# Performance work log

Hardware: AMD Instinct MI355X
Metric: run time of the kernel (lower is better)

## Reference

```python
import jax, jax.numpy as jnp
import numpy as np

DIM = 128
E = 400000
G = 512


def setup_inputs() -> dict:
    key = jax.random.key(0)
    ks = jax.random.split(key, 9)
    src = jax.random.normal(ks[0], (E, DIM), dtype=jnp.float32)
    dest = jax.random.normal(ks[1], (E, DIM), dtype=jnp.float32)
    edge_attr = jax.random.normal(ks[2], (E, DIM), dtype=jnp.float32)
    u = jax.random.normal(ks[3], (G, DIM), dtype=jnp.float32)
    batch = jnp.sort(jax.random.randint(ks[4], (E,), 0, G, dtype=jnp.int64))
    # MLP params: Linear(4*dim, dim) -> ReLU -> Linear(dim, dim)
    s1 = 1.0 / np.sqrt(4 * DIM)
    s2 = 1.0 / np.sqrt(DIM)
    W1 = jax.random.uniform(ks[5], (4 * DIM, DIM), minval=-s1, maxval=s1, dtype=jnp.float32)
    b1 = jax.random.uniform(ks[6], (DIM,), minval=-s1, maxval=s1, dtype=jnp.float32)
    W2 = jax.random.uniform(ks[7], (DIM, DIM), minval=-s2, maxval=s2, dtype=jnp.float32)
    b2 = jax.random.uniform(ks[8], (DIM,), minval=-s2, maxval=s2, dtype=jnp.float32)
    return {"src": src, "dest": dest, "edge_attr": edge_attr, "u": u,
            "batch": batch, "W1": W1, "b1": b1, "W2": W2, "b2": b2}


def reference(src, dest, edge_attr, u, batch, W1, b1, W2, b2):
    # gather global state per edge, concat 4 blocks -> [E, 4*dim]
    comb = jnp.concatenate([src, dest, edge_attr, u[batch]], axis=1)
    h = jax.nn.relu(comb @ W1 + b1)
    return h @ W2 + b2
```

## Files before the change

kernel.cpp:

```cpp
#include <hip/hip_runtime.h>

#define DIM 128

typedef __attribute__((ext_vector_type(8))) short short8;
typedef __attribute__((ext_vector_type(4))) float f32x4;

__device__ __forceinline__ unsigned short f2bf(float f) {
    union { float f; unsigned u; } v; v.f = f;
    unsigned u = v.u;
    return (unsigned short)((u + 0x7FFFu + ((u >> 16) & 1u)) >> 16);
}

__device__ __forceinline__ short8 cvt8(f32x4 lo, f32x4 hi) {
    short8 r;
    r[0] = (short)f2bf(lo[0]); r[1] = (short)f2bf(lo[1]);
    r[2] = (short)f2bf(lo[2]); r[3] = (short)f2bf(lo[3]);
    r[4] = (short)f2bf(hi[0]); r[5] = (short)f2bf(hi[1]);
    r[6] = (short)f2bf(hi[2]); r[7] = (short)f2bf(hi[3]);
    return r;
}

__global__ void prep_weights(const float* __restrict__ W1, const float* __restrict__ W2,
                             unsigned short* __restrict__ W1t, unsigned short* __restrict__ W2t) {
    int tid = blockIdx.x * blockDim.x + threadIdx.x;
    if (tid < 512 * 128) {
        int n = tid >> 9;
        int k = tid & 511;
        W1t[tid] = f2bf(W1[k * 128 + n]);
    } else if (tid < 512 * 128 + 128 * 128) {
        int t = tid - 512 * 128;
        int n = t >> 7;
        int k = t & 127;
        W2t[t] = f2bf(W2[k * 128 + n]);
    }
}

__device__ __forceinline__ void chunk_gemm(const float* p0, const float* p1,
                                           const unsigned short* __restrict__ wchunk,
                                           int quad, int l16, f32x4 acc[2][8]) {
#pragma unroll
    for (int s = 0; s < 4; ++s) {
        const int kl = s * 32 + quad * 8;
        f32x4 a0lo = *(const f32x4*)(p0 + kl);
        f32x4 a0hi = *(const f32x4*)(p0 + kl + 4);
        f32x4 a1lo = *(const f32x4*)(p1 + kl);
        f32x4 a1hi = *(const f32x4*)(p1 + kl + 4);
        short8 a0 = cvt8(a0lo, a0hi);
        short8 a1 = cvt8(a1lo, a1hi);
#pragma unroll
        for (int nt = 0; nt < 8; ++nt) {
            short8 b = *(const short8*)(wchunk + (nt * 16 + l16) * 512 + kl);
            acc[0][nt] = __builtin_amdgcn_mfma_f32_16x16x32_bf16(a0, b, acc[0][nt], 0, 0, 0);
            acc[1][nt] = __builtin_amdgcn_mfma_f32_16x16x32_bf16(a1, b, acc[1][nt], 0, 0, 0);
        }
    }
}

__global__ __launch_bounds__(256, 2)
void megnet_edge(const float* __restrict__ src, const float* __restrict__ dst,
                 const float* __restrict__ edge_attr, const float* __restrict__ u,
                 const int* __restrict__ batch,
                 const unsigned short* __restrict__ W1t, const unsigned short* __restrict__ W2t,
                 const float* __restrict__ b1, const float* __restrict__ b2,
                 float* __restrict__ out, int E) {
    __shared__ unsigned char lds_raw[4 * 32 * 256];

    const int tid  = threadIdx.x;
    const int wave = tid >> 6;
    const int lane = tid & 63;
    const int quad = lane >> 4;
    const int l16  = lane & 15;

    const long rowBase = (long)blockIdx.x * 128 + wave * 32;
    if (rowBase >= E) return;

    float b1r[8], b2r[8];
#pragma unroll
    for (int nt = 0; nt < 8; ++nt) {
        b1r[nt] = b1[nt * 16 + l16];
        b2r[nt] = b2[nt * 16 + l16];
    }

    const long ar0 = rowBase + l16;
    const long ar1 = rowBase + 16 + l16;
    const int ub0 = batch[ar0];
    const int ub1 = batch[ar1];

    f32x4 acc[2][8];
#pragma unroll
    for (int mt = 0; mt < 2; ++mt)
#pragma unroll
        for (int nt = 0; nt < 8; ++nt) acc[mt][nt] = (f32x4)0.0f;

    chunk_gemm(src + ar0 * DIM,       src + ar1 * DIM,       W1t + 0 * 128, quad, l16, acc);
    chunk_gemm(dst + ar0 * DIM,       dst + ar1 * DIM,       W1t + 1 * 128, quad, l16, acc);
    chunk_gemm(edge_attr + ar0 * DIM, edge_attr + ar1 * DIM, W1t + 2 * 128, quad, l16, acc);
    chunk_gemm(u + (long)ub0 * DIM,   u + (long)ub1 * DIM,   W1t + 3 * 128, quad, l16, acc);

    unsigned char* myLds = lds_raw + wave * 32 * 256;
#pragma unroll
    for (int mt = 0; mt < 2; ++mt)
#pragma unroll
        for (int nt = 0; nt < 8; ++nt)
#pragma unroll
            for (int r = 0; r < 4; ++r) {
                const int lr = mt * 16 + quad * 4 + r;
                const int cc = nt * 16 + l16;
                float h = acc[mt][nt][r] + b1r[nt];
                h = h > 0.0f ? h : 0.0f;
                const int g = (cc >> 3) ^ (lr & 7);
                *(unsigned short*)(myLds + lr * 256 + g * 16 + (cc & 7) * 2) = f2bf(h);
            }
    __syncthreads();

    f32x4 acc2[2][8];
#pragma unroll
    for (int mt = 0; mt < 2; ++mt)
#pragma unroll
        for (int nt = 0; nt < 8; ++nt) acc2[mt][nt] = (f32x4)0.0f;

#pragma unroll
    for (int s = 0; s < 4; ++s) {
        const int kl = s * 32 + quad * 8;
        const int g  = kl >> 3;
        const int lr0 = l16;
        const int lr1 = 16 + l16;
        short8 a0 = *(const short8*)(myLds + lr0 * 256 + ((g ^ (lr0 & 7)) * 16));
        short8 a1 = *(const short8*)(myLds + lr1 * 256 + ((g ^ (lr1 & 7)) * 16));
#pragma unroll
        for (int nt = 0; nt < 8; ++nt) {
            short8 b = *(const short8*)(W2t + (nt * 16 + l16) * 128 + kl);
            acc2[0][nt] = __builtin_amdgcn_mfma_f32_16x16x32_bf16(a0, b, acc2[0][nt], 0, 0, 0);
            acc2[1][nt] = __builtin_amdgcn_mfma_f32_16x16x32_bf16(a1, b, acc2[1][nt], 0, 0, 0);
        }
    }

#pragma unroll
    for (int mt = 0; mt < 2; ++mt)
#pragma unroll
        for (int nt = 0; nt < 8; ++nt)
#pragma unroll
            for (int r = 0; r < 4; ++r) {
                const long row = rowBase + mt * 16 + quad * 4 + r;
                const int col = nt * 16 + l16;
                out[row * DIM + col] = acc2[mt][nt][r] + b2r[nt];
            }
}

extern "C" void kernel_launch(void* const* d_in, const int* in_sizes, int n_in,
                              void* d_out, int out_size, void* d_ws, size_t ws_size,
                              hipStream_t stream) {
    const float* src       = (const float*)d_in[0];
    const float* dst       = (const float*)d_in[1];
    const float* edge_attr = (const float*)d_in[2];
    const float* u         = (const float*)d_in[3];
    const int*   batch     = (const int*)d_in[4];
    const float* W1        = (const float*)d_in[5];
    const float* b1        = (const float*)d_in[6];
    const float* W2        = (const float*)d_in[7];
    const float* b2        = (const float*)d_in[8];
    float* out             = (float*)d_out;

    unsigned short* W1t = (unsigned short*)d_ws;
    unsigned short* W2t = W1t + 512 * 128;

    const int E = in_sizes[0] / DIM;

    prep_weights<<<(512 * 128 + 128 * 128 + 255) / 256, 256, 0, stream>>>(W1, W2, W1t, W2t);
    megnet_edge<<<(E + 127) / 128, 256, 0, stream>>>(src, dst, edge_attr, u, batch,
                                                     W1t, W2t, b1, b2, out, E);
}
```

Measured before the change: 800.3 us.

## Software-pipeline activation and weight loads across GEMM chunks, drop block barrier

Restructures the first GEMM so the next input chunk's fp32 rows are prefetched into registers while the current chunk is converted and multiplied. Weight fragments are double-buffered one k-step ahead in both GEMMs. Because each wave only reads its own LDS region, the block-wide __syncthreads is replaced with a wave-local lgkmcnt wait. Bias loads are moved later to ease register pressure. The extra register buffers may raise VGPR use and risk spills under the 2-blocks-per-SIMD launch bound.

```diff
diff --git a/kernel.cpp b/kernel.cpp
--- a/kernel.cpp
+++ b/kernel.cpp
@@ -35,27 +35,6 @@
     }
 }
 
-__device__ __forceinline__ void chunk_gemm(const float* p0, const float* p1,
-                                           const unsigned short* __restrict__ wchunk,
-                                           int quad, int l16, f32x4 acc[2][8]) {
-#pragma unroll
-    for (int s = 0; s < 4; ++s) {
-        const int kl = s * 32 + quad * 8;
-        f32x4 a0lo = *(const f32x4*)(p0 + kl);
-        f32x4 a0hi = *(const f32x4*)(p0 + kl + 4);
-        f32x4 a1lo = *(const f32x4*)(p1 + kl);
-        f32x4 a1hi = *(const f32x4*)(p1 + kl + 4);
-        short8 a0 = cvt8(a0lo, a0hi);
-        short8 a1 = cvt8(a1lo, a1hi);
-#pragma unroll
-        for (int nt = 0; nt < 8; ++nt) {
-            short8 b = *(const short8*)(wchunk + (nt * 16 + l16) * 512 + kl);
-            acc[0][nt] = __builtin_amdgcn_mfma_f32_16x16x32_bf16(a0, b, acc[0][nt], 0, 0, 0);
-            acc[1][nt] = __builtin_amdgcn_mfma_f32_16x16x32_bf16(a1, b, acc[1][nt], 0, 0, 0);
-        }
-    }
-}
-
 __global__ __launch_bounds__(256, 2)
 void megnet_edge(const float* __restrict__ src, const float* __restrict__ dst,
                  const float* __restrict__ edge_attr, const float* __restrict__ u,
@@ -74,28 +53,79 @@
     const long rowBase = (long)blockIdx.x * 128 + wave * 32;
     if (rowBase >= E) return;
 
-    float b1r[8], b2r[8];
-#pragma unroll
-    for (int nt = 0; nt < 8; ++nt) {
-        b1r[nt] = b1[nt * 16 + l16];
-        b2r[nt] = b2[nt * 16 + l16];
-    }
-
     const long ar0 = rowBase + l16;
-    const long ar1 = rowBase + 16 + l16;
+    const long ar1 = ar0 + 16;
     const int ub0 = batch[ar0];
     const int ub1 = batch[ar1];
 
+    const float* rp0[4] = { src + ar0 * DIM, dst + ar0 * DIM, edge_attr + ar0 * DIM, u + (long)ub0 * DIM };
+    const float* rp1[4] = { src + ar1 * DIM, dst + ar1 * DIM, edge_attr + ar1 * DIM, u + (long)ub1 * DIM };
+
+    const int koff = quad * 8;
+
     f32x4 acc[2][8];
 #pragma unroll
     for (int mt = 0; mt < 2; ++mt)
 #pragma unroll
         for (int nt = 0; nt < 8; ++nt) acc[mt][nt] = (f32x4)0.0f;
 
-    chunk_gemm(src + ar0 * DIM,       src + ar1 * DIM,       W1t + 0 * 128, quad, l16, acc);
-    chunk_gemm(dst + ar0 * DIM,       dst + ar1 * DIM,       W1t + 1 * 128, quad, l16, acc);
-    chunk_gemm(edge_attr + ar0 * DIM, edge_attr + ar1 * DIM, W1t + 2 * 128, quad, l16, acc);
-    chunk_gemm(u + (long)ub0 * DIM,   u + (long)ub1 * DIM,   W1t + 3 * 128, quad, l16, acc);
+    f32x4 raw0[8], raw1[8];
+#pragma unroll
+    for (int j = 0; j < 8; ++j) {
+        const int off = (j >> 1) * 32 + koff + (j & 1) * 4;
+        raw0[j] = *(const f32x4*)(rp0[0] + off);
+        raw1[j] = *(const f32x4*)(rp1[0] + off);
+    }
+
+#pragma unroll
+    for (int c = 0; c < 4; ++c) {
+        short8 a0[4], a1[4];
+#pragma unroll
+        for (int s = 0; s < 4; ++s) a0[s] = cvt8(raw0[2 * s], raw0[2 * s + 1]);
+        if (c < 3) {
+#pragma unroll
+            for (int j = 0; j < 8; ++j) {
+                const int off = (j >> 1) * 32 + koff + (j & 1) * 4;
+                raw0[j] = *(const f32x4*)(rp0[c + 1] + off);
+            }
+        }
+#pragma unroll
+        for (int s = 0; s < 4; ++s) a1[s] = cvt8(raw1[2 * s], raw1[2 * s + 1]);
+        if (c < 3) {
+#pragma unroll
+            for (int j = 0; j < 8; ++j) {
+                const int off = (j >> 1) * 32 + koff + (j & 1) * 4;
+                raw1[j] = *(const f32x4*)(rp1[c + 1] + off);
+            }
+        }
+
+        const unsigned short* wc = W1t + c * 128;
+        short8 bn[8];
+#pragma unroll
+        for (int nt = 0; nt < 8; ++nt)
+            bn[nt] = *(const short8*)(wc + (nt * 16 + l16) * 512 + koff);
+
+#pragma unroll
+        for (int s = 0; s < 4; ++s) {
+            short8 bc[8];
+#pragma unroll
+            for (int nt = 0; nt < 8; ++nt) bc[nt] = bn[nt];
+            if (s < 3) {
+#pragma unroll
+                for (int nt = 0; nt < 8; ++nt)
+                    bn[nt] = *(const short8*)(wc + (nt * 16 + l16) * 512 + (s + 1) * 32 + koff);
+            }
+#pragma unroll
+            for (int nt = 0; nt < 8; ++nt) {
+                acc[0][nt] = __builtin_amdgcn_mfma_f32_16x16x32_bf16(a0[s], bc[nt], acc[0][nt], 0, 0, 0);
+                acc[1][nt] = __builtin_amdgcn_mfma_f32_16x16x32_bf16(a1[s], bc[nt], acc[1][nt], 0, 0, 0);
+            }
+        }
+    }
+
+    float b1r[8];
+#pragma unroll
+    for (int nt = 0; nt < 8; ++nt) b1r[nt] = b1[nt * 16 + l16];
 
     unsigned char* myLds = lds_raw + wave * 32 * 256;
 #pragma unroll
@@ -111,7 +141,7 @@
                 const int g = (cc >> 3) ^ (lr & 7);
                 *(unsigned short*)(myLds + lr * 256 + g * 16 + (cc & 7) * 2) = f2bf(h);
             }
-    __syncthreads();
+    asm volatile("s_waitcnt lgkmcnt(0)" ::: "memory");
 
     f32x4 acc2[2][8];
 #pragma unroll
@@ -119,21 +149,41 @@
 #pragma unroll
         for (int nt = 0; nt < 8; ++nt) acc2[mt][nt] = (f32x4)0.0f;
 
+    short8 ha0[4], ha1[4];
 #pragma unroll
     for (int s = 0; s < 4; ++s) {
-        const int kl = s * 32 + quad * 8;
-        const int g  = kl >> 3;
+        const int g = s * 4 + quad;
         const int lr0 = l16;
         const int lr1 = 16 + l16;
-        short8 a0 = *(const short8*)(myLds + lr0 * 256 + ((g ^ (lr0 & 7)) * 16));
-        short8 a1 = *(const short8*)(myLds + lr1 * 256 + ((g ^ (lr1 & 7)) * 16));
+        ha0[s] = *(const short8*)(myLds + lr0 * 256 + ((g ^ (lr0 & 7)) * 16));
+        ha1[s] = *(const short8*)(myLds + lr1 * 256 + ((g ^ (lr1 & 7)) * 16));
+    }
+
+    short8 bn2[8];
+#pragma unroll
+    for (int nt = 0; nt < 8; ++nt)
+        bn2[nt] = *(const short8*)(W2t + (nt * 16 + l16) * 128 + koff);
+
+#pragma unroll
+    for (int s = 0; s < 4; ++s) {
+        short8 bc2[8];
+#pragma unroll
+        for (int nt = 0; nt < 8; ++nt) bc2[nt] = bn2[nt];
+        if (s < 3) {
+#pragma unroll
+            for (int nt = 0; nt < 8; ++nt)
+                bn2[nt] = *(const short8*)(W2t + (nt * 16 + l16) * 128 + (s + 1) * 32 + koff);
+        }
 #pragma unroll
         for (int nt = 0; nt < 8; ++nt) {
-            short8 b = *(const short8*)(W2t + (nt * 16 + l16) * 128 + kl);
-            acc2[0][nt] = __builtin_amdgcn_mfma_f32_16x16x32_bf16(a0, b, acc2[0][nt], 0, 0, 0);
-            acc2[1][nt] = __builtin_amdgcn_mfma_f32_16x16x32_bf16(a1, b, acc2[1][nt], 0, 0, 0);
-        }
-    }
+            acc2[0][nt] = __builtin_amdgcn_mfma_f32_16x16x32_bf16(ha0[s], bc2[nt], acc2[0][nt], 0, 0, 0);
+            acc2[1][nt] = __builtin_amdgcn_mfma_f32_16x16x32_bf16(ha1[s], bc2[nt], acc2[1][nt], 0, 0, 0);
+        }
+    }
+
+    float b2r[8];
+#pragma unroll
+    for (int nt = 0; nt < 8; ++nt) b2r[nt] = b2[nt * 16 + l16];
 
 #pragma unroll
     for (int mt = 0; mt < 2; ++mt)
```

After: 799.6 us. About the same (-0.1%).
